# Kernel optimization log

Measured on AMD Instinct MI355X. Metric: run time of the kernel, lower is better.

Reference implementation:

```python
import jax, jax.numpy as jnp
import numpy as np

B, T, D_IN, H, C = 4096, 20, 300, 512, 10


def setup_inputs() -> dict:
    key = jax.random.key(0)
    ks = jax.random.split(key, 12)
    s = lambda fan_in, fan_out: float(np.sqrt(6.0 / (fan_in + fan_out)))  # xavier uniform bound
    u = lambda k, shape, b: jax.random.uniform(k, shape, jnp.float32, -b, b)
    return {
        "x": jax.random.normal(ks[0], (B, T, D_IN), jnp.float32),
        "W_emb": u(ks[1], (D_IN, H), s(D_IN, H)),
        "b_emb": jnp.zeros((H,), jnp.float32),
        "wx0": u(ks[2], (H, H), s(H, H)),
        "wh0": u(ks[3], (H, H), s(H, H)),
        "b0": jnp.zeros((H,), jnp.float32),
        "wx1": u(ks[4], (H, H), s(H, H)),
        "wh1": u(ks[5], (H, H), s(H, H)),
        "b1": jnp.zeros((H,), jnp.float32),
        "wx2": u(ks[6], (H, H), s(H, H)),
        "wh2": u(ks[7], (H, H), s(H, H)),
        "b2": jnp.zeros((H,), jnp.float32),
        "W_fc": u(ks[8], (H, C), s(H, C)),
        "b_fc": jnp.zeros((C,), jnp.float32),
    }


def reference(x, W_emb, b_emb, wx0, wh0, b0, wx1, wh1, b1, wx2, wh2, b2, W_fc, b_fc):
    # embedding_layer applied to all timesteps: [B,T,300] -> [B,T,512]
    emb = jnp.einsum("btd,dh->bth", x, W_emb) + b_emb
    h0 = jnp.zeros((x.shape[0], wx0.shape[1]), x.dtype)
    init = (h0, h0, h0)

    def step(carry, v_t):  # v_t: [B,H]
        h0, h1, h2 = carry
        h0 = jnp.tanh(v_t @ wx0 + h0 @ wh0 + b0)
        h1 = jnp.tanh(h0 @ wx1 + h1 @ wh1 + b1)
        h2 = jnp.tanh(h1 @ wx2 + h2 @ wh2 + b2)
        return (h0, h1, h2), None

    (h0, h1, h2), _ = jax.lax.scan(step, init, jnp.swapaxes(emb, 0, 1))  # scan over T
    return h2 @ W_fc + b_fc  # [B, C]
```

## Files before the change

kernel.cpp:

```cpp
#include <hip/hip_runtime.h>

typedef _Float16 f16;
typedef _Float16 f16x8 __attribute__((ext_vector_type(8)));
typedef float floatx4 __attribute__((ext_vector_type(4)));

__device__ __forceinline__ float ftanh(float x) {
  float ax = __builtin_fabsf(x);
  float e  = __expf(-2.0f * ax);
  float t  = (1.0f - e) * __builtin_amdgcn_rcpf(1.0f + e);
  return x < 0.0f ? -t : t;
}

__device__ __forceinline__ void gll16(const f16* g, f16* l) {
  __builtin_amdgcn_global_load_lds(
      (const __attribute__((address_space(1))) void*)g,
      (__attribute__((address_space(3))) void*)l, 16, 0, 0);
}

template<int FJ>
__device__ __forceinline__ void tile_gemm(
    const f16* __restrict__ A0, int ldA0,
    const f16* __restrict__ A1, int ldA1,
    int K, const f16* __restrict__ WT,
    const float* __restrict__ bias,
    f16* __restrict__ outp, int bm, int bn, f16* sm)
{
  const int tid  = threadIdx.x;
  const int w    = tid >> 6;
  const int lane = tid & 63;
  const int lm   = lane & 15;
  const int quad = lane >> 4;
  const int wm   = (w >> 1) * 64;
  const int wn   = (w & 1) * (FJ * 16);
  const int srow8 = lane >> 3;
  const int scol  = ((lane & 7) ^ srow8) * 8;
  const int lmx   = lane & 7;
  constexpr int SB = 8192 + FJ * 2048;

  floatx4 acc[4][FJ];
  #pragma unroll
  for (int i = 0; i < 4; ++i)
    #pragma unroll
    for (int j = 0; j < FJ; ++j)
      acc[i][j] = (floatx4){0.f, 0.f, 0.f, 0.f};

  auto stage = [&](int buf, int k0) {
    const f16* Asrc = (k0 < 512) ? (A0 + k0) : (A1 + (k0 - 512));
    const int  ld   = (k0 < 512) ? ldA0 : ldA1;
    f16* As0 = sm + buf * SB;
    f16* Ws0 = As0 + 8192;
    #pragma unroll
    for (int i = 0; i < 4; ++i) {
      int r = (w * 4 + i) * 8 + srow8;
      gll16(Asrc + (size_t)(bm + r) * ld + scol, As0 + (w * 4 + i) * 512);
    }
    #pragma unroll
    for (int i = 0; i < FJ; ++i) {
      int r = (w * FJ + i) * 8 + srow8;
      gll16(WT + (size_t)(bn + r) * K + k0 + scol, Ws0 + (w * FJ + i) * 512);
    }
  };

  const int NS = K >> 6;
  stage(0, 0);
  __syncthreads();
  for (int s = 0; s < NS; ++s) {
    if (s + 1 < NS) stage((s + 1) & 1, (s + 1) << 6);
    const f16* As0 = sm + (s & 1) * SB;
    const f16* Ws0 = As0 + 8192;
    #pragma unroll
    for (int kk = 0; kk < 64; kk += 32) {
      const int sw = (((kk >> 3) + quad) ^ lmx) << 3;
      f16x8 a[4], bfr[FJ];
      #pragma unroll
      for (int fi = 0; fi < 4; ++fi)
        a[fi] = *(const f16x8*)&As0[(size_t)(wm + fi * 16 + lm) * 64 + sw];
      #pragma unroll
      for (int fj = 0; fj < FJ; ++fj)
        bfr[fj] = *(const f16x8*)&Ws0[(size_t)(wn + fj * 16 + lm) * 64 + sw];
      __builtin_amdgcn_s_setprio(1);
      #pragma unroll
      for (int fi = 0; fi < 4; ++fi)
        #pragma unroll
        for (int fj = 0; fj < FJ; ++fj)
          acc[fi][fj] = __builtin_amdgcn_mfma_f32_16x16x32_f16(a[fi], bfr[fj], acc[fi][fj], 0, 0, 0);
      __builtin_amdgcn_s_setprio(0);
    }
    __syncthreads();
  }

  constexpr int ES = FJ * 32 + 8;
  #pragma unroll
  for (int fi = 0; fi < 4; ++fi)
    #pragma unroll
    for (int fj = 0; fj < FJ; ++fj) {
      int col = wn + fj * 16 + lm;
      #pragma unroll
      for (int r = 0; r < 4; ++r) {
        int row = wm + fi * 16 + quad * 4 + r;
        sm[row * ES + col] = (f16)acc[fi][fj][r];
      }
    }
  __syncthreads();
  constexpr int TPR = (FJ * 32) / 8;
  constexpr int RPP = 256 / TPR;
  #pragma unroll
  for (int p = 0; p < 128 / RPP; ++p) {
    int row = p * RPP + tid / TPR;
    int c8  = (tid % TPR) * 8;
    f16x8 ve = *(const f16x8*)&sm[row * ES + c8];
    floatx4 bv0 = *(const floatx4*)&bias[bn + c8];
    floatx4 bv1 = *(const floatx4*)&bias[bn + c8 + 4];
    union { f16 e[8]; f16x8 v; } o;
    #pragma unroll
    for (int j = 0; j < 4; ++j) o.e[j]     = (f16)ftanh((float)ve[j]     + bv0[j]);
    #pragma unroll
    for (int j = 0; j < 4; ++j) o.e[4 + j] = (f16)ftanh((float)ve[4 + j] + bv1[j]);
    *(f16x8*)(outp + (size_t)(bm + row) * 512 + bn + c8) = o.v;
  }
}

__global__ __launch_bounds__(256, 2)
void rnn_step(int wv, const f16* __restrict__ xh,
              const f16* __restrict__ W0T, const f16* __restrict__ W1T,
              const f16* __restrict__ W2T,
              const float* __restrict__ bcomb, const float* __restrict__ b1,
              const float* __restrict__ b2,
              const f16* __restrict__ H0c, f16* __restrict__ H0n,
              const f16* __restrict__ H1c, f16* __restrict__ H1n,
              const f16* __restrict__ H2c, f16* __restrict__ H2n)
{
  __shared__ f16 sm[32768];
  const int b   = blockIdx.x;
  const int xcd = b & 7;
  const int r   = b >> 3;

  if (r < 32) {
    if (wv > 19) return;
    const int slab = xcd * 4 + (r & 3);
    const int bn   = (r >> 2) * 64;
    tile_gemm<2>(H0c, 512, xh + (size_t)wv * 320, 6400, 832, W0T, bcomb,
                 H0n, slab * 128, bn, sm);
  } else if (r < 48) {
    if (wv < 1 || wv > 20) return;
    const int rr   = r - 32;
    const int slab = xcd * 4 + (rr & 3);
    const int bn   = (rr >> 2) * 128;
    tile_gemm<4>(H0c, 512, H1c, 512, 1024, W1T, b1, H1n, slab * 128, bn, sm);
  } else {
    if (wv < 2) return;
    const int rr   = r - 48;
    const int slab = xcd * 4 + (rr & 3);
    const int bn   = (rr >> 2) * 128;
    tile_gemm<4>(H1c, 512, H2c, 512, 1024, W2T, b2, H2n, slab * 128, bn, sm);
  }
}

#define PX_N 1600

__global__ __launch_bounds__(256)
void prep_x(const float* __restrict__ x, f16* __restrict__ xh)
{
  const int NTH = PX_N * 256;
  const int g = blockIdx.x * 256 + threadIdx.x;
  floatx4 va[8], vb[8];
  int rw[8], cc[8];
  const floatx4 z4 = {0.f, 0.f, 0.f, 0.f};
  #pragma unroll
  for (int s = 0; s < 8; ++s) {
    int U = g + s * NTH;
    int row = U / 40;
    int c   = (U - row * 40) * 8;
    rw[s] = row; cc[s] = c;
    const float* src = x + (size_t)row * 300 + c;
    va[s] = (c + 4 <= 300) ? *(const floatx4*)src : z4;
    vb[s] = (c + 8 <= 300) ? *(const floatx4*)(src + 4) : z4;
  }
  #pragma unroll
  for (int s = 0; s < 8; ++s) {
    union { f16 e[8]; f16x8 v; } t;
    #pragma unroll
    for (int j = 0; j < 4; ++j) { t.e[j] = (f16)va[s][j]; t.e[4 + j] = (f16)vb[s][j]; }
    *(f16x8*)(xh + (size_t)rw[s] * 320 + cc[s]) = t.v;
  }
}

#define QW_WCE 640
#define QW_BC  648
#define QW_WT  1288
#define QW_Z   4360

__global__ __launch_bounds__(256)
void prep_w(const float* __restrict__ W_emb, const float* __restrict__ b_emb,
            const float* __restrict__ wx0, const float* __restrict__ wh0,
            const float* __restrict__ b0,
            const float* __restrict__ wx1, const float* __restrict__ wh1,
            const float* __restrict__ wx2, const float* __restrict__ wh2,
            f16* __restrict__ W0T, f16* __restrict__ W1T, f16* __restrict__ W2T,
            float* __restrict__ bcomb,
            f16* __restrict__ H0a, f16* __restrict__ H1b, f16* __restrict__ H2a)
{
  __shared__ float smem[16384];
  const int b   = blockIdx.x;
  const int tid = threadIdx.x;
  const floatx4 z4 = {0.f, 0.f, 0.f, 0.f};

  if (b < QW_WCE) {
    float* wes = smem;
    float* wxs = smem + 8192;
    const int kt = b >> 5, nt = b & 31;
    const int k0 = kt * 16, n0 = nt * 16;
    const int rr = tid >> 4, cc = tid & 15;
    {
      const int k = k0 + rr;
      #pragma unroll
      for (int q = 0; q < 8; ++q) {
        floatx4 v = (k < 300) ? *(const floatx4*)&W_emb[(size_t)k * 512 + cc * 32 + q * 4] : z4;
        *(floatx4*)&wes[rr * 512 + cc * 32 + q * 4] = v;
      }
    }
    #pragma unroll 4
    for (int jj = 0; jj < 32; ++jj) {
      int j = rr * 32 + jj;
      wxs[j * 16 + cc] = wx0[(size_t)j * 512 + n0 + cc];
    }
    __syncthreads();
    float s = 0.f;
    #pragma unroll 8
    for (int j = 0; j < 512; ++j)
      s = __builtin_fmaf(wes[rr * 512 + j], wxs[j * 16 + cc], s);
    W0T[(size_t)(n0 + cc) * 832 + 512 + k0 + rr] = (f16)s;
  } else if (b < QW_BC) {
    float* red = smem;
    int n     = (b - QW_WCE) * 64 + (tid & 63);
    int chunk = tid >> 6;
    float s = 0.f;
    const float* be = b_emb + chunk * 128;
    const float* wx = wx0 + (size_t)(chunk * 128) * 512 + n;
    #pragma unroll 4
    for (int j = 0; j < 128; ++j)
      s = __builtin_fmaf(be[j], wx[(size_t)j * 512], s);
    red[tid] = s;
    __syncthreads();
    if (chunk == 0)
      bcomb[n] = b0[n] + red[tid] + red[tid + 64] + red[tid + 128] + red[tid + 192];
  } else if (b < QW_WT) {
    int id = (b - QW_BC) * 256 + tid;
    if (id < 32768) {
      int n = id & 511, k8 = id >> 9;
      union { f16 e[8]; f16x8 v; } t;
      #pragma unroll
      for (int j = 0; j < 8; ++j) t.e[j] = (f16)wh0[(size_t)(k8 * 8 + j) * 512 + n];
      *(f16x8*)&W0T[(size_t)n * 832 + k8 * 8] = t.v;
    } else if (id < 98304) {
      int i2 = id - 32768;
      int n = i2 & 511, k8 = i2 >> 9;
      union { f16 e[8]; f16x8 v; } t;
      const float* src = (k8 < 64) ? (wx1 + (size_t)(k8 * 8) * 512 + n)
                                   : (wh1 + (size_t)((k8 - 64) * 8) * 512 + n);
      #pragma unroll
      for (int j = 0; j < 8; ++j) t.e[j] = (f16)src[(size_t)j * 512];
      *(f16x8*)&W1T[(size_t)n * 1024 + k8 * 8] = t.v;
    } else {
      int i2 = id - 98304;
      int n = i2 & 511, k8 = i2 >> 9;
      union { f16 e[8]; f16x8 v; } t;
      const float* src = (k8 < 64) ? (wx2 + (size_t)(k8 * 8) * 512 + n)
                                   : (wh2 + (size_t)((k8 - 64) * 8) * 512 + n);
      #pragma unroll
      for (int j = 0; j < 8; ++j) t.e[j] = (f16)src[(size_t)j * 512];
      *(f16x8*)&W2T[(size_t)n * 1024 + k8 * 8] = t.v;
    }
  } else {
    int id = (b - QW_WT) * 256 + tid;
    f16x8 z8 = {};
    f16* dst = (id < 262144) ? H0a : (id < 524288) ? H1b : H2a;
    *(f16x8*)(dst + (size_t)(id & 262143) * 8) = z8;
  }
}

__global__ void fc_kernel(const f16* __restrict__ h2,
                          const float* __restrict__ Wfc, const float* __restrict__ bfc,
                          float* __restrict__ out)
{
  __shared__ float wf[5120];
  __shared__ float bf[16];
  const int tid = threadIdx.x;
  for (int i = tid; i < 5120; i += 256) wf[i] = Wfc[i];
  if (tid < 10) bf[tid] = bfc[tid];
  __syncthreads();
  int id = blockIdx.x * 256 + tid;
  int row = id / 10;
  int c = id - row * 10;
  float s = bf[c];
  const f16* hr = h2 + (size_t)row * 512;
  for (int k8 = 0; k8 < 64; ++k8) {
    f16x8 h8 = *(const f16x8*)(hr + k8 * 8);
    #pragma unroll
    for (int j = 0; j < 8; ++j)
      s = __builtin_fmaf((float)h8[j], wf[(k8 * 8 + j) * 10 + c], s);
  }
  out[id] = s;
}

extern "C" void kernel_launch(void* const* d_in, const int* in_sizes, int n_in,
                              void* d_out, int out_size, void* d_ws, size_t ws_size,
                              hipStream_t stream)
{
  (void)in_sizes; (void)n_in; (void)out_size; (void)ws_size;
  const float* x     = (const float*)d_in[0];
  const float* W_emb = (const float*)d_in[1];
  const float* b_emb = (const float*)d_in[2];
  const float* wx0   = (const float*)d_in[3];
  const float* wh0   = (const float*)d_in[4];
  const float* b0    = (const float*)d_in[5];
  const float* wx1   = (const float*)d_in[6];
  const float* wh1   = (const float*)d_in[7];
  const float* b1    = (const float*)d_in[8];
  const float* wx2   = (const float*)d_in[9];
  const float* wh2   = (const float*)d_in[10];
  const float* b2    = (const float*)d_in[11];
  const float* W_fc  = (const float*)d_in[12];
  const float* b_fc  = (const float*)d_in[13];
  float* out = (float*)d_out;

  char* ws = (char*)d_ws;
  size_t off = 0;
  auto alloc = [&](size_t bytes) -> void* {
    void* p = ws + off;
    off = (off + bytes + 255) & ~(size_t)255;
    return p;
  };
  f16*   xh    = (f16*)alloc((size_t)81920 * 320 * 2);
  f16*   W0T   = (f16*)alloc((size_t)512 * 832 * 2);
  f16*   W1T   = (f16*)alloc((size_t)512 * 1024 * 2);
  f16*   W2T   = (f16*)alloc((size_t)512 * 1024 * 2);
  float* bcomb = (float*)alloc(512 * 4);
  f16*   H0a   = (f16*)alloc((size_t)4096 * 512 * 2);
  f16*   H0b   = (f16*)alloc((size_t)4096 * 512 * 2);
  f16*   H1a   = (f16*)alloc((size_t)4096 * 512 * 2);
  f16*   H1b   = (f16*)alloc((size_t)4096 * 512 * 2);
  f16*   H2a   = (f16*)alloc((size_t)4096 * 512 * 2);
  f16*   H2b   = (f16*)alloc((size_t)4096 * 512 * 2);

  prep_x<<<PX_N, 256, 0, stream>>>(x, xh);
  prep_w<<<QW_Z, 256, 0, stream>>>(W_emb, b_emb, wx0, wh0, b0,
                                   wx1, wh1, wx2, wh2,
                                   W0T, W1T, W2T, bcomb, H0a, H1b, H2a);

  for (int wv = 0; wv < 22; ++wv) {
    const int cur = wv & 1;
    f16* H0c = cur ? H0b : H0a;  f16* H0n = cur ? H0a : H0b;
    f16* H1c = cur ? H1b : H1a;  f16* H1n = cur ? H1a : H1b;
    f16* H2c = cur ? H2b : H2a;  f16* H2n = cur ? H2a : H2b;
    rnn_step<<<512, 256, 0, stream>>>(wv, xh, W0T, W1T, W2T, bcomb, b1, b2,
                                      H0c, H0n, H1c, H1n, H2c, H2n);
  }

  fc_kernel<<<160, 256, 0, stream>>>(H2a, W_fc, b_fc, out);
}
```

Measured before the change: 553.0 us.

## Precompute layer-0 input projection for all timesteps in one batched GEMM

Moves the x·(W_emb·wx0) contribution out of the per-step recurrent kernel into a single large GEMM over all 81920 rows. Its output U is stored in fp16, and each layer-0 step then adds U to its h0·wh0 product before tanh. Layer-0 step K drops from 832 to 512, which shortens the critical-path wave GEMMs. In exchange it adds a large batched GEMM plus an 80 MB intermediate write and reread, and rounds the pre-activation input to fp16.

```diff
diff --git a/kernel.cpp b/kernel.cpp
--- a/kernel.cpp
+++ b/kernel.cpp
@@ -17,12 +17,13 @@
       (__attribute__((address_space(3))) void*)l, 16, 0, 0);
 }
 
-template<int FJ>
+template<int FJ, bool TANH, bool ADDU>
 __device__ __forceinline__ void tile_gemm(
     const f16* __restrict__ A0, int ldA0,
     const f16* __restrict__ A1, int ldA1,
     int K, const f16* __restrict__ WT,
     const float* __restrict__ bias,
+    const f16* __restrict__ addp, int ldadd,
     f16* __restrict__ outp, int bm, int bn, f16* sm)
 {
   const int tid  = threadIdx.x;
@@ -109,23 +110,48 @@
     int row = p * RPP + tid / TPR;
     int c8  = (tid % TPR) * 8;
     f16x8 ve = *(const f16x8*)&sm[row * ES + c8];
-    floatx4 bv0 = *(const floatx4*)&bias[bn + c8];
-    floatx4 bv1 = *(const floatx4*)&bias[bn + c8 + 4];
     union { f16 e[8]; f16x8 v; } o;
-    #pragma unroll
-    for (int j = 0; j < 4; ++j) o.e[j]     = (f16)ftanh((float)ve[j]     + bv0[j]);
-    #pragma unroll
-    for (int j = 0; j < 4; ++j) o.e[4 + j] = (f16)ftanh((float)ve[4 + j] + bv1[j]);
+    if constexpr (ADDU) {
+      f16x8 u8 = *(const f16x8*)&addp[(size_t)(bm + row) * ldadd + bn + c8];
+      #pragma unroll
+      for (int j = 0; j < 8; ++j)
+        o.e[j] = (f16)ftanh((float)ve[j] + (float)u8[j]);
+    } else {
+      floatx4 bv0 = *(const floatx4*)&bias[bn + c8];
+      floatx4 bv1 = *(const floatx4*)&bias[bn + c8 + 4];
+      if constexpr (TANH) {
+        #pragma unroll
+        for (int j = 0; j < 4; ++j) o.e[j]     = (f16)ftanh((float)ve[j]     + bv0[j]);
+        #pragma unroll
+        for (int j = 0; j < 4; ++j) o.e[4 + j] = (f16)ftanh((float)ve[4 + j] + bv1[j]);
+      } else {
+        #pragma unroll
+        for (int j = 0; j < 4; ++j) o.e[j]     = (f16)((float)ve[j]     + bv0[j]);
+        #pragma unroll
+        for (int j = 0; j < 4; ++j) o.e[4 + j] = (f16)((float)ve[4 + j] + bv1[j]);
+      }
+    }
     *(f16x8*)(outp + (size_t)(bm + row) * 512 + bn + c8) = o.v;
   }
 }
 
 __global__ __launch_bounds__(256, 2)
-void rnn_step(int wv, const f16* __restrict__ xh,
+void ugemm(const f16* __restrict__ xh, const f16* __restrict__ WceT,
+           const float* __restrict__ bcomb, f16* __restrict__ U)
+{
+  __shared__ f16 sm[32768];
+  const int b  = blockIdx.x;
+  const int bm = (b >> 2) * 128;
+  const int bn = (b & 3) * 128;
+  tile_gemm<4, false, false>(xh, 320, xh, 320, 320, WceT, bcomb, nullptr, 0,
+                             U, bm, bn, sm);
+}
+
+__global__ __launch_bounds__(256, 2)
+void rnn_step(int wv, const f16* __restrict__ U,
               const f16* __restrict__ W0T, const f16* __restrict__ W1T,
               const f16* __restrict__ W2T,
-              const float* __restrict__ bcomb, const float* __restrict__ b1,
-              const float* __restrict__ b2,
+              const float* __restrict__ b1, const float* __restrict__ b2,
               const f16* __restrict__ H0c, f16* __restrict__ H0n,
               const f16* __restrict__ H1c, f16* __restrict__ H1n,
               const f16* __restrict__ H2c, f16* __restrict__ H2n)
@@ -139,20 +165,23 @@
     if (wv > 19) return;
     const int slab = xcd * 4 + (r & 3);
     const int bn   = (r >> 2) * 64;
-    tile_gemm<2>(H0c, 512, xh + (size_t)wv * 320, 6400, 832, W0T, bcomb,
-                 H0n, slab * 128, bn, sm);
+    tile_gemm<2, true, true>(H0c, 512, H0c, 512, 512, W0T, nullptr,
+                             U + (size_t)wv * 512, 20 * 512,
+                             H0n, slab * 128, bn, sm);
   } else if (r < 48) {
     if (wv < 1 || wv > 20) return;
     const int rr   = r - 32;
     const int slab = xcd * 4 + (rr & 3);
     const int bn   = (rr >> 2) * 128;
-    tile_gemm<4>(H0c, 512, H1c, 512, 1024, W1T, b1, H1n, slab * 128, bn, sm);
+    tile_gemm<4, true, false>(H0c, 512, H1c, 512, 1024, W1T, b1, nullptr, 0,
+                              H1n, slab * 128, bn, sm);
   } else {
     if (wv < 2) return;
     const int rr   = r - 48;
     const int slab = xcd * 4 + (rr & 3);
     const int bn   = (rr >> 2) * 128;
-    tile_gemm<4>(H1c, 512, H2c, 512, 1024, W2T, b2, H2n, slab * 128, bn, sm);
+    tile_gemm<4, true, false>(H1c, 512, H2c, 512, 1024, W2T, b2, nullptr, 0,
+                              H2n, slab * 128, bn, sm);
   }
 }
 
@@ -196,7 +225,8 @@
             const float* __restrict__ b0,
             const float* __restrict__ wx1, const float* __restrict__ wh1,
             const float* __restrict__ wx2, const float* __restrict__ wh2,
-            f16* __restrict__ W0T, f16* __restrict__ W1T, f16* __restrict__ W2T,
+            f16* __restrict__ WceT, f16* __restrict__ W0T,
+            f16* __restrict__ W1T, f16* __restrict__ W2T,
             float* __restrict__ bcomb,
             f16* __restrict__ H0a, f16* __restrict__ H1b, f16* __restrict__ H2a)
 {
@@ -229,7 +259,7 @@
     #pragma unroll 8
     for (int j = 0; j < 512; ++j)
       s = __builtin_fmaf(wes[rr * 512 + j], wxs[j * 16 + cc], s);
-    W0T[(size_t)(n0 + cc) * 832 + 512 + k0 + rr] = (f16)s;
+    WceT[(size_t)(n0 + cc) * 320 + k0 + rr] = (f16)s;
   } else if (b < QW_BC) {
     float* red = smem;
     int n     = (b - QW_WCE) * 64 + (tid & 63);
@@ -251,7 +281,7 @@
       union { f16 e[8]; f16x8 v; } t;
       #pragma unroll
       for (int j = 0; j < 8; ++j) t.e[j] = (f16)wh0[(size_t)(k8 * 8 + j) * 512 + n];
-      *(f16x8*)&W0T[(size_t)n * 832 + k8 * 8] = t.v;
+      *(f16x8*)&W0T[(size_t)n * 512 + k8 * 8] = t.v;
     } else if (id < 98304) {
       int i2 = id - 32768;
       int n = i2 & 511, k8 = i2 >> 9;
@@ -332,7 +362,9 @@
     return p;
   };
   f16*   xh    = (f16*)alloc((size_t)81920 * 320 * 2);
-  f16*   W0T   = (f16*)alloc((size_t)512 * 832 * 2);
+  f16*   U     = (f16*)alloc((size_t)81920 * 512 * 2);
+  f16*   WceT  = (f16*)alloc((size_t)512 * 320 * 2);
+  f16*   W0T   = (f16*)alloc((size_t)512 * 512 * 2);
   f16*   W1T   = (f16*)alloc((size_t)512 * 1024 * 2);
   f16*   W2T   = (f16*)alloc((size_t)512 * 1024 * 2);
   float* bcomb = (float*)alloc(512 * 4);
@@ -346,14 +378,16 @@
   prep_x<<<PX_N, 256, 0, stream>>>(x, xh);
   prep_w<<<QW_Z, 256, 0, stream>>>(W_emb, b_emb, wx0, wh0, b0,
                                    wx1, wh1, wx2, wh2,
-                                   W0T, W1T, W2T, bcomb, H0a, H1b, H2a);
+                                   WceT, W0T, W1T, W2T, bcomb, H0a, H1b, H2a);
+
+  ugemm<<<2560, 256, 0, stream>>>(xh, WceT, bcomb, U);
 
   for (int wv = 0; wv < 22; ++wv) {
     const int cur = wv & 1;
     f16* H0c = cur ? H0b : H0a;  f16* H0n = cur ? H0a : H0b;
     f16* H1c = cur ? H1b : H1a;  f16* H1n = cur ? H1a : H1b;
     f16* H2c = cur ? H2b : H2a;  f16* H2n = cur ? H2a : H2b;
-    rnn_step<<<512, 256, 0, stream>>>(wv, xh, W0T, W1T, W2T, bcomb, b1, b2,
+    rnn_step<<<512, 256, 0, stream>>>(wv, U, W0T, W1T, W2T, b1, b2,
                                       H0c, H0n, H1c, H1n, H2c, H2n);
   }
 
```

Result: slower. 616.4 us (+11.5%).
